# Kernel tuning notes

Hardware: AMD Instinct MI355X
Metric: run time of the kernel (lower is better)

The kernel has to match this reference:

```python
import jax, jax.numpy as jnp
import numpy as np
from jax import lax

DIM = 64
DSTATE = 16
EXPAND = 2
DINNER = DIM * EXPAND
DTRANK = (DIM + 15) // 16  # ceil(d_model/16) = 4
B, D, H, W = 1, 24, 24, 24
EPS = 1e-5


def setup_inputs() -> dict:
    key = jax.random.key(0)
    ks = jax.random.split(key, 40)
    def nrm(i, shape, s=0.02):
        return jax.random.normal(ks[i], shape, jnp.float32) * s
    inp = {}
    inp['x'] = jax.random.normal(ks[0], (B, DIM, D, H, W), jnp.float32)
    # three directional view convs + instance-norm affine params
    inp['w1'] = nrm(1, (DIM, DIM, 3, 1, 1)); inp['b1'] = jnp.zeros((DIM,), jnp.float32)
    inp['g1'] = jnp.ones((DIM,), jnp.float32) + nrm(2, (DIM,)); inp['be1'] = nrm(3, (DIM,))
    inp['w2'] = nrm(4, (DIM, DIM, 1, 3, 1)); inp['b2'] = jnp.zeros((DIM,), jnp.float32)
    inp['g2'] = jnp.ones((DIM,), jnp.float32) + nrm(5, (DIM,)); inp['be2'] = nrm(6, (DIM,))
    inp['w3'] = nrm(7, (DIM, DIM, 1, 1, 3)); inp['b3'] = jnp.zeros((DIM,), jnp.float32)
    inp['g3'] = jnp.ones((DIM,), jnp.float32) + nrm(8, (DIM,)); inp['be3'] = nrm(9, (DIM,))
    # MambaUnit layernorm
    inp['ln_w'] = jnp.ones((DIM,), jnp.float32); inp['ln_b'] = jnp.zeros((DIM,), jnp.float32)
    # Mamba params (shared across the three views, as in the source)
    inp['in_proj_w'] = nrm(10, (2 * DINNER, DIM))
    inp['conv_w'] = jnp.ones((DINNER,), jnp.float32) + nrm(11, (DINNER,))  # d_conv=1 depthwise
    inp['conv_b'] = nrm(12, (DINNER,))
    inp['x_proj_w'] = nrm(13, (DTRANK + 2 * DSTATE, DINNER))
    inp['dt_w'] = nrm(14, (DINNER, DTRANK), 0.1)
    inp['dt_b'] = nrm(15, (DINNER,), 0.1)
    inp['A_log'] = jnp.log(jnp.tile(jnp.arange(1, DSTATE + 1, dtype=jnp.float32), (DINNER, 1)))
    inp['D_param'] = jnp.ones((DINNER,), jnp.float32)
    inp['out_proj_w'] = nrm(16, (DIM, DINNER))
    # fusion 1x1x1 conv + instance norm
    inp['wf'] = nrm(17, (DIM, 3 * DIM, 1, 1, 1)); inp['bf'] = jnp.zeros((DIM,), jnp.float32)
    inp['gf'] = jnp.ones((DIM,), jnp.float32) + nrm(18, (DIM,)); inp['bef'] = nrm(19, (DIM,))
    return inp


def silu(x):
    return x * jax.nn.sigmoid(x)


def conv3d(x, w, b, pad):
    out = lax.conv_general_dilated(
        x, w, (1, 1, 1), [(pad[0], pad[0]), (pad[1], pad[1]), (pad[2], pad[2])],
        dimension_numbers=('NCDHW', 'OIDHW', 'NCDHW'))
    return out + b[None, :, None, None, None]


def instance_norm(x, g, b):
    m = x.mean(axis=(2, 3, 4), keepdims=True)
    v = x.var(axis=(2, 3, 4), keepdims=True)  # biased, as in torch InstanceNorm
    return (x - m) / jnp.sqrt(v + EPS) * g[None, :, None, None, None] + b[None, :, None, None, None]


def layer_norm(x, g, b):
    m = x.mean(axis=-1, keepdims=True)
    v = x.var(axis=-1, keepdims=True)
    return (x - m) / jnp.sqrt(v + EPS) * g + b


def mamba(u, in_proj_w, conv_w, conv_b, x_proj_w, dt_w, dt_b, A_log, D_param, out_proj_w):
    # u: (B, L, d_model)
    xz = u @ in_proj_w.T                       # (B, L, 2*DINNER)
    xi, z = jnp.split(xz, 2, axis=-1)
    xi = silu(xi * conv_w + conv_b)            # d_conv=1 depthwise conv == per-channel affine
    xdbl = xi @ x_proj_w.T                     # (B, L, DTRANK + 2*DSTATE)
    dt = xdbl[..., :DTRANK]
    Bm = xdbl[..., DTRANK:DTRANK + DSTATE]
    Cm = xdbl[..., DTRANK + DSTATE:]
    dt = jax.nn.softplus(dt @ dt_w.T + dt_b)   # (B, L, DINNER)
    A = -jnp.exp(A_log)                        # (DINNER, DSTATE)
    dA = jnp.exp(dt[..., None] * A)            # (B, L, DINNER, DSTATE)
    dBx = dt[..., None] * Bm[:, :, None, :] * xi[..., None]
    def comb(c1, c2):
        a1, b1 = c1
        a2, b2 = c2
        return a1 * a2, a2 * b1 + b2
    _, h = lax.associative_scan(comb, (dA, dBx), axis=1)  # h: (B, L, DINNER, DSTATE)
    y = jnp.einsum('blin,bln->bli', h, Cm) + xi * D_param
    y = y * silu(z)
    return y @ out_proj_w.T


def mamba_unit(x5, ln_w, ln_b, mparams):
    Bb, C = x5.shape[:2]
    dims = x5.shape[2:]
    xf = jnp.transpose(x5.reshape(Bb, C, -1), (0, 2, 1))  # (B, L, C)
    xn = layer_norm(xf, ln_w, ln_b)
    y = mamba(xn, *mparams)
    return jnp.transpose(y, (0, 2, 1)).reshape(Bb, C, *dims)


def reference(x, w1, b1, g1, be1, w2, b2, g2, be2, w3, b3, g3, be3, ln_w, ln_b,
              in_proj_w, conv_w, conv_b, x_proj_w, dt_w, dt_b, A_log, D_param, out_proj_w,
              wf, bf, gf, bef):
    mparams = (in_proj_w, conv_w, conv_b, x_proj_w, dt_w, dt_b, A_log, D_param, out_proj_w)
    v1 = jax.nn.relu(instance_norm(conv3d(x, w1, b1, (1, 0, 0)), g1, be1))
    v2 = jax.nn.relu(instance_norm(conv3d(x, w2, b2, (0, 1, 0)), g2, be2))
    v3 = jax.nn.relu(instance_norm(conv3d(x, w3, b3, (0, 0, 1)), g3, be3))
    m1 = mamba_unit(v1, ln_w, ln_b, mparams)
    m2 = mamba_unit(v2, ln_w, ln_b, mparams)
    m3 = mamba_unit(v3, ln_w, ln_b, mparams)
    cat = jnp.concatenate([m1, m2, m3], axis=1)
    out = jax.nn.relu(instance_norm(conv3d(cat, wf, bf, (0, 0, 0)), gf, bef))
    return out
```

## Files before the change

kernel.cpp:

```cpp
#include <hip/hip_runtime.h>

#define LTOT 13824
#define NCH 108
#define CHL 128
#define EPSF 1e-5f

static const size_t OFF_U   = 1024;
static const size_t NU      = (size_t)3*LTOT*64;
static const size_t NXI     = (size_t)3*LTOT*128;
static const size_t NBM     = (size_t)3*LTOT*16;
static const size_t NAG     = (size_t)3*NCH*128*16;
static const size_t OFF_XIT = OFF_U   + NU;
static const size_t OFF_SZT = OFF_XIT + NXI;
static const size_t OFF_DTT = OFF_SZT + NXI;
static const size_t OFF_BMT = OFF_DTT + NXI;
static const size_t OFF_CMT = OFF_BMT + NBM;
static const size_t OFF_W2  = OFF_CMT + NBM;
static const size_t OFF_WT  = OFF_W2 + 24576;
static const size_t OFF_WI  = OFF_WT + 36864;
static const size_t OFF_AGA = OFF_U;
static const size_t OFF_AGB = OFF_U + NAG;
static const size_t OFF_SEED= OFF_U + 2*NAG;
static const size_t OFF_FIN = OFF_DTT;

__device__ __forceinline__ float sigm(float x){ return 1.f/(1.f+__expf(-x)); }
__device__ __forceinline__ float siluf(float x){ return x*sigm(x); }
__device__ __forceinline__ float softplusf(float x){
    return fmaxf(x,0.f) + log1pf(__expf(-fabsf(x)));
}

template<int CTRL>
__device__ __forceinline__ float dpp_add(float x){
    int v = __builtin_amdgcn_update_dpp(0, __float_as_int(x), CTRL, 0xf, 0xf, true);
    return x + __int_as_float(v);
}
__device__ __forceinline__ float sum16(float x){
    x = dpp_add<0xB1>(x);
    x = dpp_add<0x4E>(x);
    x = dpp_add<0x141>(x);
    x = dpp_add<0x140>(x);
    return x;
}

__global__ __launch_bounds__(256) void k_prep(const float* __restrict__ w1,
                      const float* __restrict__ w2, const float* __restrict__ w3,
                      const float* __restrict__ opw, const float* __restrict__ wf,
                      const float* __restrict__ ipw,
                      float* __restrict__ wt, float* __restrict__ w2t,
                      float* __restrict__ wi)
{
    if (blockIdx.x < 144){
        int idx = blockIdx.x*256 + threadIdx.x;
        int r = idx / 12288, rem = idx % 12288;
        int k = rem >> 6, o = rem & 63;
        const float* W = (r==0)?w1:(r==1)?w2:w3;
        wt[idx] = W[o*192 + k];
    } else if (blockIdx.x < 240){
        int idx = (blockIdx.x-144)*256 + threadIdx.x;
        int o = idx & 63, ri = idx >> 6;
        int r = ri >> 7, i = ri & 127;
        float acc = 0.f;
        for (int c2=0;c2<64;c2++)
            acc += opw[c2*128+i] * wf[o*192 + r*64 + c2];
        w2t[idx] = acc;
    } else {
        int idx = (blockIdx.x-240)*256 + threadIdx.x;
        int col = idx & 255, q = idx >> 8;
        wi[q*256 + col] = ipw[col*64 + q];
    }
}

__global__ __launch_bounds__(192) void k_conv(const float* __restrict__ x,
                       const float* __restrict__ wt,
                       const float* __restrict__ b1, const float* __restrict__ b2,
                       const float* __restrict__ b3,
                       float* __restrict__ u, float* __restrict__ ws)
{
    __shared__ __align__(16) float xs[1152];
    __shared__ __align__(16) float wl[48*64];
    __shared__ float ssum[64], ssq[64];
    const int r = blockIdx.y;
    const int row = blockIdx.x;
    const float* Bz = (r==0)?b1:(r==1)?b2:b3;
    const int tid = threadIdx.x;

    if (tid < 64){ ssum[tid]=0.f; ssq[tid]=0.f; }

    const int og = tid & 15, wg = tid >> 4;
    const int o0 = og*4, w0 = wg*2;
    float acc[4][2];
    {
        float b0 = Bz[o0], b1v = Bz[o0+1], b2v = Bz[o0+2], b3v = Bz[o0+3];
        acc[0][0]=b0;  acc[0][1]=b0;
        acc[1][0]=b1v; acc[1][1]=b1v;
        acc[2][0]=b2v; acc[2][1]=b2v;
        acc[3][0]=b3v; acc[3][1]=b3v;
    }

    const float* wtr = wt + (size_t)r*12288;
    const int d = row/24, h = row%24;

    for (int ph=0; ph<4; ph++){
        __syncthreads();
        for (int s = tid; s < 3072; s += 192)
            wl[s] = wtr[ph*3072 + s];
        for (int s = tid; s < 1152; s += 192){
            int w = s % 24; int kt = s / 24; int ic2 = kt/3, t = kt%3;
            int ic = ph*16 + ic2;
            int src = 0; bool valid = true;
            if (r==0){ int dd = d+t-1; valid = (dd>=0 && dd<24); src = (dd*24+h)*24 + w; }
            else if (r==1){ int hh = h+t-1; valid = (hh>=0 && hh<24); src = (d*24+hh)*24 + w; }
            else { int ww = w+t-1; valid = (ww>=0 && ww<24); src = row*24 + ww; }
            xs[s] = valid ? x[(size_t)ic*LTOT + src] : 0.f;
        }
        __syncthreads();
        for (int ic2=0; ic2<16; ic2++){
            #pragma unroll
            for (int t=0;t<3;t++){
                float4 wv = *(const float4*)&wl[(ic2*3+t)*64 + o0];
                float2 xv = *(const float2*)&xs[(ic2*3+t)*24 + w0];
                acc[0][0]=fmaf(wv.x,xv.x,acc[0][0]); acc[0][1]=fmaf(wv.x,xv.y,acc[0][1]);
                acc[1][0]=fmaf(wv.y,xv.x,acc[1][0]); acc[1][1]=fmaf(wv.y,xv.y,acc[1][1]);
                acc[2][0]=fmaf(wv.z,xv.x,acc[2][0]); acc[2][1]=fmaf(wv.z,xv.y,acc[2][1]);
                acc[3][0]=fmaf(wv.w,xv.x,acc[3][0]); acc[3][1]=fmaf(wv.w,xv.y,acc[3][1]);
            }
        }
    }

    size_t ub = ((size_t)r*LTOT + (size_t)row*24)*64;
    float ps[4], pq[4];
    #pragma unroll
    for (int wj=0; wj<2; wj++){
        float4 v = make_float4(acc[0][wj],acc[1][wj],acc[2][wj],acc[3][wj]);
        *(float4*)&u[ub + (size_t)(w0+wj)*64 + o0] = v;
        if (wj==0){ ps[0]=v.x; pq[0]=v.x*v.x; ps[1]=v.y; pq[1]=v.y*v.y;
                    ps[2]=v.z; pq[2]=v.z*v.z; ps[3]=v.w; pq[3]=v.w*v.w; }
        else { ps[0]+=v.x; pq[0]+=v.x*v.x; ps[1]+=v.y; pq[1]+=v.y*v.y;
               ps[2]+=v.z; pq[2]+=v.z*v.z; ps[3]+=v.w; pq[3]+=v.w*v.w; }
    }
    #pragma unroll
    for (int oj=0;oj<4;oj++){
        atomicAdd(&ssum[o0+oj], ps[oj]);
        atomicAdd(&ssq[o0+oj], pq[oj]);
    }
    __syncthreads();
    if (tid < 64){
        atomicAdd(&ws[r*64 + tid], ssum[tid]);
        atomicAdd(&ws[192 + r*64 + tid], ssq[tid]);
    }
}

__global__ __launch_bounds__(192) void k_stats1(float* ws){
    int t = threadIdx.x;
    float s = ws[t], q = ws[192+t];
    float m = s*(1.f/(float)LTOT);
    float v = q*(1.f/(float)LTOT) - m*m;
    ws[512+t] = m; ws[704+t] = rsqrtf(v + EPSF);
}

__global__ __launch_bounds__(256, 4) void k_inproj(const float* __restrict__ u, float* __restrict__ xiT,
                         float* __restrict__ szT, const float* __restrict__ wi,
                         const float* __restrict__ cw, const float* __restrict__ cb,
                         const float* __restrict__ ws,
                         const float* g1,const float* be1,const float* g2,const float* be2,
                         const float* g3,const float* be3,
                         const float* lnw,const float* lnb)
{
    __shared__ float xl[64*65];
    const int tid = threadIdx.x, r = blockIdx.y;
    const int lane = tid & 63;
    const int wv = __builtin_amdgcn_readfirstlane(tid >> 6);
    const int l0 = blockIdx.x*64;
    size_t gbase = (size_t)r*LTOT + l0;

    {
        const float* g  = (r==0)?g1:(r==1)?g2:g3;
        const float* be = (r==0)?be1:(r==1)?be2:be3;
        float m  = ws[512 + r*64 + lane], rs = ws[704 + r*64 + lane];
        float gg = g[lane], bb = be[lane];
        float lw = lnw[lane], lb = lnb[lane];
        for (int j=0;j<16;j++){
            int p = wv*16 + j;
            float vv = u[(gbase+p)*64 + lane];
            vv = fmaxf((vv-m)*rs*gg + bb, 0.f);
            float s1 = sum16(vv), s2 = sum16(vv*vv);
            s1 += __shfl_xor(s1,16); s2 += __shfl_xor(s2,16);
            s1 += __shfl_xor(s1,32); s2 += __shfl_xor(s2,32);
            float mean = s1*(1.f/64.f);
            float var  = s2*(1.f/64.f) - mean*mean;
            xl[lane*65 + p] = (vv-mean)*rsqrtf(var+EPSF)*lw + lb;
        }
    }
    __syncthreads();

    float acc[64];
    #pragma unroll
    for (int j=0;j<64;j++) acc[j] = 0.f;
    const float* wbase = wi + wv*64;
    for (int q=0;q<64;q++){
        float xq = xl[q*65 + lane];
        const float* wq = wbase + q*256;
        #pragma unroll
        for (int j=0;j<64;j++)
            acc[j] = fmaf(wq[j], xq, acc[j]);
    }

    const bool isx = (wv < 2);
    float* dst = isx ? xiT : szT;
    const int c0 = (wv & 1)*64;
    #pragma unroll
    for (int j=0;j<64;j++){
        int c2 = c0 + j;
        float v;
        if (isx) v = siluf(fmaf(acc[j], cw[c2], cb[c2]));
        else     v = siluf(acc[j]);
        dst[((size_t)r*128 + c2)*LTOT + l0 + lane] = v;
    }
}

__global__ __launch_bounds__(256) void k_xproj(const float* __restrict__ xiT, float* __restrict__ dtT,
                        float* __restrict__ BmT, float* __restrict__ CmT,
                        const float* __restrict__ xpw, const float* __restrict__ dtw,
                        const float* __restrict__ dtb)
{
    __shared__ __align__(16) float xt[128*36];
    __shared__ float ww[36*129];
    __shared__ float sd[4*36];
    const int tid = threadIdx.x, r = blockIdx.y;
    const int l0 = blockIdx.x*32;

    for (int s = tid; s < 4096; s += 256){
        int c = s>>5, p = s&31;
        xt[c*36+p] = xiT[((size_t)r*128 + c)*LTOT + l0 + p];
    }
    for (int s = tid; s < 4608; s += 256){
        int k = s>>7, c = s&127;
        ww[k*129+c] = xpw[s];
    }
    __syncthreads();

    const int wv = tid>>6, lane = tid&63;
    float acc[8] = {0,0,0,0,0,0,0,0};
    if (lane < 36){
        const float* wrow = &ww[lane*129];
        for (int c=0;c<128;c++){
            float w = wrow[c];
            float4 a = *(const float4*)&xt[c*36 + wv*8];
            float4 b = *(const float4*)&xt[c*36 + wv*8 + 4];
            acc[0]=fmaf(w,a.x,acc[0]); acc[1]=fmaf(w,a.y,acc[1]);
            acc[2]=fmaf(w,a.z,acc[2]); acc[3]=fmaf(w,a.w,acc[3]);
            acc[4]=fmaf(w,b.x,acc[4]); acc[5]=fmaf(w,b.y,acc[5]);
            acc[6]=fmaf(w,b.z,acc[6]); acc[7]=fmaf(w,b.w,acc[7]);
        }
    }
    if (lane>=4 && lane<36){
        float* dst = (lane<20) ? BmT : CmT;
        int n = (lane<20) ? (lane-4) : (lane-20);
        size_t base = ((size_t)r*16 + n)*LTOT + l0 + wv*8;
        *(float4*)&dst[base]   = make_float4(acc[0],acc[1],acc[2],acc[3]);
        *(float4*)&dst[base+4] = make_float4(acc[4],acc[5],acc[6],acc[7]);
    }
    if (lane < 4){
        #pragma unroll
        for (int p=0;p<8;p++) sd[lane*36 + wv*8 + p] = acc[p];
    }
    __syncthreads();

    const int i = tid>>1, ph = tid&1;
    float4 dw = *(const float4*)&dtw[i*4];
    float db = dtb[i];
    float buf[16];
    #pragma unroll
    for (int t=0;t<16;t++){
        int p = ph*16 + t;
        float v = db + dw.x*sd[0*36+p] + dw.y*sd[1*36+p]
                     + dw.z*sd[2*36+p] + dw.w*sd[3*36+p];
        buf[t] = softplusf(v);
    }
    size_t base = ((size_t)r*128 + i)*LTOT + l0 + ph*16;
    #pragma unroll
    for (int q=0;q<4;q++){
        *(float4*)&dtT[base + 4*q] =
            make_float4(buf[4*q], buf[4*q+1], buf[4*q+2], buf[4*q+3]);
    }
}

__global__ __launch_bounds__(256) void k_scan1(const float* __restrict__ dtT, const float* __restrict__ BmT,
                        const float* __restrict__ xiT, const float* __restrict__ Alog,
                        float* __restrict__ aga, float* __restrict__ agb)
{
    __shared__ __align__(16) float sdt[64*68];
    __shared__ __align__(16) float sxi[64*68];
    __shared__ __align__(16) float sbm[16*68];
    const int tid = threadIdx.x;
    const int ng = tid & 3, il = tid >> 2;
    const int c = blockIdx.x, ib = blockIdx.y, r = blockIdx.z;
    const int i = ib*64 + il;

    float A2[4];
    #pragma unroll
    for (int k=0;k<4;k++) A2[k] = -expf(Alog[i*16 + ng*4 + k]) * 1.44269504f;

    const size_t rowDX = ((size_t)r*128 + ib*64)*LTOT + (size_t)c*CHL;
    const size_t rowB  = ((size_t)r*16)*LTOT + (size_t)c*CHL;

    float b0=0.f,b1=0.f,b2=0.f,b3=0.f, dsum=0.f;

    for (int hh=0; hh<2; hh++){
        __syncthreads();
        const int lb = hh*64;
        for (int f = tid; f < 1024; f += 256){
            int row = f >> 4, t4 = f & 15;
            *(float4*)&sdt[row*68 + t4*4] = *(const float4*)&dtT[rowDX + (size_t)row*LTOT + lb + t4*4];
            *(float4*)&sxi[row*68 + t4*4] = *(const float4*)&xiT[rowDX + (size_t)row*LTOT + lb + t4*4];
        }
        for (int f = tid; f < 256; f += 256){
            int row = f >> 4, t4 = f & 15;
            *(float4*)&sbm[row*68 + t4*4] = *(const float4*)&BmT[rowB + (size_t)row*LTOT + lb + t4*4];
        }
        __syncthreads();

        for (int t4 = 0; t4 < 16; t4++){
            float4 d4 = *(const float4*)&sdt[il*68 + t4*4];
            float4 x4 = *(const float4*)&sxi[il*68 + t4*4];
            float4 B0 = *(const float4*)&sbm[(ng*4+0)*68 + t4*4];
            float4 B1 = *(const float4*)&sbm[(ng*4+1)*68 + t4*4];
            float4 B2 = *(const float4*)&sbm[(ng*4+2)*68 + t4*4];
            float4 B3 = *(const float4*)&sbm[(ng*4+3)*68 + t4*4];
            #define S1Q(dv,xv,c0,c1,c2,c3) { \
                float dx = (dv)*(xv); dsum += (dv); \
                b0 = fmaf(exp2f(A2[0]*(dv)), b0, dx*(c0)); \
                b1 = fmaf(exp2f(A2[1]*(dv)), b1, dx*(c1)); \
                b2 = fmaf(exp2f(A2[2]*(dv)), b2, dx*(c2)); \
                b3 = fmaf(exp2f(A2[3]*(dv)), b3, dx*(c3)); }
            S1Q(d4.x, x4.x, B0.x, B1.x, B2.x, B3.x)
            S1Q(d4.y, x4.y, B0.y, B1.y, B2.y, B3.y)
            S1Q(d4.z, x4.z, B0.z, B1.z, B2.z, B3.z)
            S1Q(d4.w, x4.w, B0.w, B1.w, B2.w, B3.w)
            #undef S1Q
        }
    }

    size_t o = ((size_t)(r*NCH+c)*128 + i)*16 + ng*4;
    *(float4*)&aga[o] = make_float4(exp2f(A2[0]*dsum), exp2f(A2[1]*dsum),
                                    exp2f(A2[2]*dsum), exp2f(A2[3]*dsum));
    *(float4*)&agb[o] = make_float4(b0,b1,b2,b3);
}

__global__ __launch_bounds__(512) void k_scan2(const float* __restrict__ aga, const float* __restrict__ agb,
                        float* __restrict__ seed)
{
    int t = blockIdx.x*512 + threadIdx.x;
    int r = t >> 11, rem = t & 2047;
    float h = 0.f;
    for (int c=0;c<NCH;c++){
        size_t idx = (size_t)(r*NCH+c)*2048 + rem;
        float a = aga[idx], b = agb[idx];
        seed[idx] = h;
        h = fmaf(a, h, b);
    }
}

__global__ __launch_bounds__(256) void k_scan3(const float* __restrict__ dtT, const float* __restrict__ BmT,
                        const float* __restrict__ CmT, const float* __restrict__ xiT,
                        float* __restrict__ szT, const float* __restrict__ Alog,
                        const float* __restrict__ Dp, const float* __restrict__ seed)
{
    __shared__ __align__(16) float sdt[64*68];
    __shared__ __align__(16) float sxi[64*68];
    __shared__ __align__(16) float sbm[16*68];
    __shared__ __align__(16) float scm[16*68];
    const int tid = threadIdx.x;
    const int ng = tid & 3, il = tid >> 2;
    const int c = blockIdx.x, ib = blockIdx.y, r = blockIdx.z;
    const int i = ib*64 + il;

    float A2[4];
    #pragma unroll
    for (int k=0;k<4;k++) A2[k] = -expf(Alog[i*16 + ng*4 + k]) * 1.44269504f;
    const float Dv = Dp[i];

    float4 h4 = *(const float4*)&seed[((size_t)(r*NCH+c)*128 + i)*16 + ng*4];
    float h0=h4.x, h1=h4.y, h2=h4.z, h3=h4.w;

    const size_t rowDX = ((size_t)r*128 + ib*64)*LTOT + (size_t)c*CHL;
    const size_t rowB  = ((size_t)r*16)*LTOT + (size_t)c*CHL;

    for (int hh=0; hh<2; hh++){
        __syncthreads();
        const int lb = hh*64;
        for (int f = tid; f < 1024; f += 256){
            int row = f >> 4, t4 = f & 15;
            *(float4*)&sdt[row*68 + t4*4] = *(const float4*)&dtT[rowDX + (size_t)row*LTOT + lb + t4*4];
            *(float4*)&sxi[row*68 + t4*4] = *(const float4*)&xiT[rowDX + (size_t)row*LTOT + lb + t4*4];
        }
        for (int f = tid; f < 512; f += 256){
            int half = f >> 8, f2 = f & 255;
            int row = f2 >> 4, t4 = f2 & 15;
            if (half == 0)
                *(float4*)&sbm[row*68 + t4*4] = *(const float4*)&BmT[rowB + (size_t)row*LTOT + lb + t4*4];
            else
                *(float4*)&scm[row*68 + t4*4] = *(const float4*)&CmT[rowB + (size_t)row*LTOT + lb + t4*4];
        }
        __syncthreads();

        for (int t4 = 0; t4 < 16; t4++){
            float4 d4 = *(const float4*)&sdt[il*68 + t4*4];
            float4 x4 = *(const float4*)&sxi[il*68 + t4*4];
            float4 B0 = *(const float4*)&sbm[(ng*4+0)*68 + t4*4];
            float4 B1 = *(const float4*)&sbm[(ng*4+1)*68 + t4*4];
            float4 B2 = *(const float4*)&sbm[(ng*4+2)*68 + t4*4];
            float4 B3 = *(const float4*)&sbm[(ng*4+3)*68 + t4*4];
            float4 C0 = *(const float4*)&scm[(ng*4+0)*68 + t4*4];
            float4 C1 = *(const float4*)&scm[(ng*4+1)*68 + t4*4];
            float4 C2 = *(const float4*)&scm[(ng*4+2)*68 + t4*4];
            float4 C3 = *(const float4*)&scm[(ng*4+3)*68 + t4*4];
            float4 y4;
            #define S3Q(dv,xv,b0c,b1c,b2c,b3c,c0c,c1c,c2c,c3c,oy) { \
                float dx = (dv)*(xv); \
                h0 = fmaf(exp2f(A2[0]*(dv)), h0, dx*(b0c)); \
                h1 = fmaf(exp2f(A2[1]*(dv)), h1, dx*(b1c)); \
                h2 = fmaf(exp2f(A2[2]*(dv)), h2, dx*(b2c)); \
                h3 = fmaf(exp2f(A2[3]*(dv)), h3, dx*(b3c)); \
                float p = h0*(c0c); p = fmaf(h1,(c1c),p); \
                p = fmaf(h2,(c2c),p); p = fmaf(h3,(c3c),p); \
                p = dpp_add<0xB1>(p); p = dpp_add<0x4E>(p); \
                oy = fmaf((xv), Dv, p); }
            S3Q(d4.x,x4.x, B0.x,B1.x,B2.x,B3.x, C0.x,C1.x,C2.x,C3.x, y4.x)
            S3Q(d4.y,x4.y, B0.y,B1.y,B2.y,B3.y, C0.y,C1.y,C2.y,C3.y, y4.y)
            S3Q(d4.z,x4.z, B0.z,B1.z,B2.z,B3.z, C0.z,C1.z,C2.z,C3.z, y4.z)
            S3Q(d4.w,x4.w, B0.w,B1.w,B2.w,B3.w, C0.w,C1.w,C2.w,C3.w, y4.w)
            #undef S3Q
            if (ng == 0) *(float4*)&sdt[il*68 + t4*4] = y4;
        }
        __syncthreads();

        for (int f = tid; f < 1024; f += 256){
            int row = f >> 4, t4 = f & 15;
            size_t gidx = rowDX + (size_t)row*LTOT + lb + t4*4;
            float4 yv = *(const float4*)&sdt[row*68 + t4*4];
            float4 s  = *(const float4*)&szT[gidx];
            *(float4*)&szT[gidx] = make_float4(yv.x*s.x, yv.y*s.y, yv.z*s.z, yv.w*s.w);
        }
    }
}

__global__ __launch_bounds__(256, 1) void k_fin(const float* __restrict__ yT, const float* __restrict__ w2t,
                      const float* __restrict__ bfb, float* __restrict__ fin,
                      float* __restrict__ ws)
{
    __shared__ __align__(16) float yl[384*20];
    __shared__ float part[4*16*64];
    __shared__ float ssum[64], ssq[64];
    const int tid = threadIdx.x;
    const int l0 = blockIdx.x*16;
    const int o = tid & 63, sg = tid >> 6;

    for (int f = tid; f < 6144; f += 256){
        int k = f >> 4, p = f & 15;
        yl[k*20 + p] = yT[(size_t)k*LTOT + l0 + p];
    }
    float wreg[96];
    {
        const float* wp = w2t + (size_t)(sg*96)*64 + o;
        #pragma unroll
        for (int j=0;j<96;j++) wreg[j] = wp[(size_t)j*64];
    }
    if (tid < 64){ ssum[tid]=0.f; ssq[tid]=0.f; }
    __syncthreads();

    float acc[16];
    #pragma unroll
    for (int p=0;p<16;p++) acc[p]=0.f;
    const float* ylbase = &yl[sg*96*20];
    #pragma unroll
    for (int j=0;j<96;j++){
        float w = wreg[j];
        const float4* yp4 = (const float4*)&ylbase[j*20];
        float4 a = yp4[0], b = yp4[1], c = yp4[2], d = yp4[3];
        acc[0] =fmaf(w,a.x,acc[0]);  acc[1] =fmaf(w,a.y,acc[1]);
        acc[2] =fmaf(w,a.z,acc[2]);  acc[3] =fmaf(w,a.w,acc[3]);
        acc[4] =fmaf(w,b.x,acc[4]);  acc[5] =fmaf(w,b.y,acc[5]);
        acc[6] =fmaf(w,b.z,acc[6]);  acc[7] =fmaf(w,b.w,acc[7]);
        acc[8] =fmaf(w,c.x,acc[8]);  acc[9] =fmaf(w,c.y,acc[9]);
        acc[10]=fmaf(w,c.z,acc[10]); acc[11]=fmaf(w,c.w,acc[11]);
        acc[12]=fmaf(w,d.x,acc[12]); acc[13]=fmaf(w,d.y,acc[13]);
        acc[14]=fmaf(w,d.z,acc[14]); acc[15]=fmaf(w,d.w,acc[15]);
    }
    #pragma unroll
    for (int p=0;p<16;p++) part[(sg*16+p)*64 + o] = acc[p];
    __syncthreads();

    float bias = bfb[o];
    float ps=0.f, pq=0.f;
    #pragma unroll
    for (int j=0;j<4;j++){
        int p = sg + j*4;
        float s = part[(0*16+p)*64+o] + part[(1*16+p)*64+o]
                + part[(2*16+p)*64+o] + part[(3*16+p)*64+o] + bias;
        fin[(size_t)(l0+p)*64 + o] = s;
        ps += s; pq += s*s;
    }
    atomicAdd(&ssum[o], ps); atomicAdd(&ssq[o], pq);
    __syncthreads();
    if (tid<64){
        atomicAdd(&ws[384+tid], ssum[tid]);
        atomicAdd(&ws[448+tid], ssq[tid]);
    }
}

__global__ __launch_bounds__(64) void k_statsF(float* ws){
    int t = threadIdx.x;
    float s = ws[384+t], q = ws[448+t];
    float m = s*(1.f/(float)LTOT);
    float v = q*(1.f/(float)LTOT) - m*m;
    ws[896+t] = m; ws[960+t] = rsqrtf(v + EPSF);
}

__global__ __launch_bounds__(256) void k_out(const float* __restrict__ fin, const float* __restrict__ ws,
                      const float* __restrict__ gf, const float* __restrict__ bef,
                      float* __restrict__ out)
{
    __shared__ float tl[64*65];
    const int tid = threadIdx.x;
    const int l0 = blockIdx.x*64;
    for (int s=tid; s<4096; s+=256){
        int li = s>>6, o = s&63;
        float v = fin[(size_t)(l0+li)*64 + o];
        v = fmaxf((v - ws[896+o])*ws[960+o]*gf[o] + bef[o], 0.f);
        tl[o*65+li] = v;
    }
    __syncthreads();
    for (int s=tid; s<4096; s+=256){
        int o = s>>6, li = s&63;
        out[(size_t)o*LTOT + l0 + li] = tl[o*65+li];
    }
}

extern "C" void kernel_launch(void* const* d_in, const int* in_sizes, int n_in,
                              void* d_out, int out_size, void* d_ws, size_t ws_size,
                              hipStream_t stream)
{
    const float* X    = (const float*)d_in[0];
    const float* W1   = (const float*)d_in[1];  const float* B1  = (const float*)d_in[2];
    const float* G1   = (const float*)d_in[3];  const float* BE1 = (const float*)d_in[4];
    const float* W2   = (const float*)d_in[5];  const float* B2  = (const float*)d_in[6];
    const float* G2   = (const float*)d_in[7];  const float* BE2 = (const float*)d_in[8];
    const float* W3   = (const float*)d_in[9];  const float* B3  = (const float*)d_in[10];
    const float* G3   = (const float*)d_in[11]; const float* BE3 = (const float*)d_in[12];
    const float* LNW  = (const float*)d_in[13]; const float* LNB = (const float*)d_in[14];
    const float* IPW  = (const float*)d_in[15];
    const float* CW   = (const float*)d_in[16]; const float* CB  = (const float*)d_in[17];
    const float* XPW  = (const float*)d_in[18];
    const float* DTW  = (const float*)d_in[19]; const float* DTB = (const float*)d_in[20];
    const float* ALOG = (const float*)d_in[21]; const float* DP  = (const float*)d_in[22];
    const float* OPW  = (const float*)d_in[23];
    const float* WF   = (const float*)d_in[24]; const float* BF  = (const float*)d_in[25];
    const float* GF   = (const float*)d_in[26]; const float* BEF = (const float*)d_in[27];
    float* ws = (float*)d_ws;

    (void)hipMemsetAsync(d_ws, 0, 2048, stream);

    k_prep  <<<304, 256, 0, stream>>>(W1, W2, W3, OPW, WF, IPW,
                                      ws+OFF_WT, ws+OFF_W2, ws+OFF_WI);
    k_conv  <<<dim3(576,3), 192, 0, stream>>>(X, ws+OFF_WT, B1, B2, B3, ws+OFF_U, ws);
    k_stats1<<<1, 192, 0, stream>>>(ws);
    k_inproj<<<dim3(216,3), 256, 0, stream>>>(ws+OFF_U, ws+OFF_XIT, ws+OFF_SZT,
                                              ws+OFF_WI, CW, CB, ws,
                                              G1,BE1,G2,BE2,G3,BE3, LNW,LNB);
    k_xproj <<<dim3(432,3), 256, 0, stream>>>(ws+OFF_XIT, ws+OFF_DTT, ws+OFF_BMT,
                                              ws+OFF_CMT, XPW, DTW, DTB);
    k_scan1 <<<dim3(NCH,2,3), 256, 0, stream>>>(ws+OFF_DTT, ws+OFF_BMT, ws+OFF_XIT,
                                                ALOG, ws+OFF_AGA, ws+OFF_AGB);
    k_scan2 <<<12, 512, 0, stream>>>(ws+OFF_AGA, ws+OFF_AGB, ws+OFF_SEED);
    k_scan3 <<<dim3(NCH,2,3), 256, 0, stream>>>(ws+OFF_DTT, ws+OFF_BMT, ws+OFF_CMT,
                                                ws+OFF_XIT, ws+OFF_SZT, ALOG, DP,
                                                ws+OFF_SEED);
    k_fin   <<<864, 256, 0, stream>>>(ws+OFF_SZT, ws+OFF_W2, BF, ws+OFF_FIN, ws);
    k_statsF<<<1, 64, 0, stream>>>(ws);
    k_out   <<<216, 256, 0, stream>>>(ws+OFF_FIN, ws, GF, BEF, (float*)d_out);
}
```

Baseline: 378.3 us.

## Process four rows per conv block with 8x4 register tiles

The directional conv kernel now has each 192-thread block handle four output rows instead of one. Each thread computes an 8-channel by 4-position register tile, which cuts the grid from 576x3 to 144x3 blocks. This amortizes the per-block weight staging into LDS across four rows and raises FMA work per LDS load. In exchange LDS use and register pressure grow, a launch-bounds occupancy hint is added, and far fewer blocks are available to fill the GPU.

```diff
diff --git a/kernel.cpp b/kernel.cpp
--- a/kernel.cpp
+++ b/kernel.cpp
@@ -70,76 +70,97 @@
     }
 }
 
-__global__ __launch_bounds__(192) void k_conv(const float* __restrict__ x,
+__global__ __launch_bounds__(192, 3) void k_conv(const float* __restrict__ x,
                        const float* __restrict__ wt,
                        const float* __restrict__ b1, const float* __restrict__ b2,
                        const float* __restrict__ b3,
                        float* __restrict__ u, float* __restrict__ ws)
 {
-    __shared__ __align__(16) float xs[1152];
+    __shared__ __align__(16) float xs[4*1152];
     __shared__ __align__(16) float wl[48*64];
     __shared__ float ssum[64], ssq[64];
     const int r = blockIdx.y;
-    const int row = blockIdx.x;
+    const int row0 = blockIdx.x*4;
     const float* Bz = (r==0)?b1:(r==1)?b2:b3;
     const int tid = threadIdx.x;
 
     if (tid < 64){ ssum[tid]=0.f; ssq[tid]=0.f; }
 
-    const int og = tid & 15, wg = tid >> 4;
-    const int o0 = og*4, w0 = wg*2;
-    float acc[4][2];
-    {
-        float b0 = Bz[o0], b1v = Bz[o0+1], b2v = Bz[o0+2], b3v = Bz[o0+3];
-        acc[0][0]=b0;  acc[0][1]=b0;
-        acc[1][0]=b1v; acc[1][1]=b1v;
-        acc[2][0]=b2v; acc[2][1]=b2v;
-        acc[3][0]=b3v; acc[3][1]=b3v;
+    const int rw = tid / 48, t2 = tid % 48;
+    const int og = t2 & 7, wg = t2 >> 3;
+    const int o0 = og*8, w0 = wg*4;
+    const int row = row0 + rw;
+    float acc[8][4];
+    #pragma unroll
+    for (int oj=0;oj<8;oj++){
+        float b = Bz[o0+oj];
+        acc[oj][0]=b; acc[oj][1]=b; acc[oj][2]=b; acc[oj][3]=b;
     }
 
     const float* wtr = wt + (size_t)r*12288;
-    const int d = row/24, h = row%24;
+    const float* xrow = &xs[rw*1152];
 
     for (int ph=0; ph<4; ph++){
         __syncthreads();
         for (int s = tid; s < 3072; s += 192)
             wl[s] = wtr[ph*3072 + s];
-        for (int s = tid; s < 1152; s += 192){
+        for (int f = tid; f < 4608; f += 192){
+            int rw2 = f / 1152, s = f % 1152;
             int w = s % 24; int kt = s / 24; int ic2 = kt/3, t = kt%3;
             int ic = ph*16 + ic2;
+            int rr = row0 + rw2;
+            int d = rr/24, h = rr%24;
             int src = 0; bool valid = true;
             if (r==0){ int dd = d+t-1; valid = (dd>=0 && dd<24); src = (dd*24+h)*24 + w; }
             else if (r==1){ int hh = h+t-1; valid = (hh>=0 && hh<24); src = (d*24+hh)*24 + w; }
-            else { int ww = w+t-1; valid = (ww>=0 && ww<24); src = row*24 + ww; }
-            xs[s] = valid ? x[(size_t)ic*LTOT + src] : 0.f;
+            else { int ww = w+t-1; valid = (ww>=0 && ww<24); src = rr*24 + ww; }
+            xs[rw2*1152 + s] = valid ? x[(size_t)ic*LTOT + src] : 0.f;
         }
         __syncthreads();
         for (int ic2=0; ic2<16; ic2++){
             #pragma unroll
             for (int t=0;t<3;t++){
-                float4 wv = *(const float4*)&wl[(ic2*3+t)*64 + o0];
-                float2 xv = *(const float2*)&xs[(ic2*3+t)*24 + w0];
-                acc[0][0]=fmaf(wv.x,xv.x,acc[0][0]); acc[0][1]=fmaf(wv.x,xv.y,acc[0][1]);
-                acc[1][0]=fmaf(wv.y,xv.x,acc[1][0]); acc[1][1]=fmaf(wv.y,xv.y,acc[1][1]);
-                acc[2][0]=fmaf(wv.z,xv.x,acc[2][0]); acc[2][1]=fmaf(wv.z,xv.y,acc[2][1]);
-                acc[3][0]=fmaf(wv.w,xv.x,acc[3][0]); acc[3][1]=fmaf(wv.w,xv.y,acc[3][1]);
+                const int kk = ic2*3+t;
+                float4 wa = *(const float4*)&wl[kk*64 + o0];
+                float4 wb = *(const float4*)&wl[kk*64 + o0 + 4];
+                float4 xv = *(const float4*)&xrow[kk*24 + w0];
+                acc[0][0]=fmaf(wa.x,xv.x,acc[0][0]); acc[0][1]=fmaf(wa.x,xv.y,acc[0][1]);
+                acc[0][2]=fmaf(wa.x,xv.z,acc[0][2]); acc[0][3]=fmaf(wa.x,xv.w,acc[0][3]);
+                acc[1][0]=fmaf(wa.y,xv.x,acc[1][0]); acc[1][1]=fmaf(wa.y,xv.y,acc[1][1]);
+                acc[1][2]=fmaf(wa.y,xv.z,acc[1][2]); acc[1][3]=fmaf(wa.y,xv.w,acc[1][3]);
+                acc[2][0]=fmaf(wa.z,xv.x,acc[2][0]); acc[2][1]=fmaf(wa.z,xv.y,acc[2][1]);
+                acc[2][2]=fmaf(wa.z,xv.z,acc[2][2]); acc[2][3]=fmaf(wa.z,xv.w,acc[2][3]);
+                acc[3][0]=fmaf(wa.w,xv.x,acc[3][0]); acc[3][1]=fmaf(wa.w,xv.y,acc[3][1]);
+                acc[3][2]=fmaf(wa.w,xv.z,acc[3][2]); acc[3][3]=fmaf(wa.w,xv.w,acc[3][3]);
+                acc[4][0]=fmaf(wb.x,xv.x,acc[4][0]); acc[4][1]=fmaf(wb.x,xv.y,acc[4][1]);
+                acc[4][2]=fmaf(wb.x,xv.z,acc[4][2]); acc[4][3]=fmaf(wb.x,xv.w,acc[4][3]);
+                acc[5][0]=fmaf(wb.y,xv.x,acc[5][0]); acc[5][1]=fmaf(wb.y,xv.y,acc[5][1]);
+                acc[5][2]=fmaf(wb.y,xv.z,acc[5][2]); acc[5][3]=fmaf(wb.y,xv.w,acc[5][3]);
+                acc[6][0]=fmaf(wb.z,xv.x,acc[6][0]); acc[6][1]=fmaf(wb.z,xv.y,acc[6][1]);
+                acc[6][2]=fmaf(wb.z,xv.z,acc[6][2]); acc[6][3]=fmaf(wb.z,xv.w,acc[6][3]);
+                acc[7][0]=fmaf(wb.w,xv.x,acc[7][0]); acc[7][1]=fmaf(wb.w,xv.y,acc[7][1]);
+                acc[7][2]=fmaf(wb.w,xv.z,acc[7][2]); acc[7][3]=fmaf(wb.w,xv.w,acc[7][3]);
             }
         }
     }
 
     size_t ub = ((size_t)r*LTOT + (size_t)row*24)*64;
-    float ps[4], pq[4];
-    #pragma unroll
-    for (int wj=0; wj<2; wj++){
-        float4 v = make_float4(acc[0][wj],acc[1][wj],acc[2][wj],acc[3][wj]);
-        *(float4*)&u[ub + (size_t)(w0+wj)*64 + o0] = v;
-        if (wj==0){ ps[0]=v.x; pq[0]=v.x*v.x; ps[1]=v.y; pq[1]=v.y*v.y;
-                    ps[2]=v.z; pq[2]=v.z*v.z; ps[3]=v.w; pq[3]=v.w*v.w; }
-        else { ps[0]+=v.x; pq[0]+=v.x*v.x; ps[1]+=v.y; pq[1]+=v.y*v.y;
-               ps[2]+=v.z; pq[2]+=v.z*v.z; ps[3]+=v.w; pq[3]+=v.w*v.w; }
-    }
-    #pragma unroll
-    for (int oj=0;oj<4;oj++){
+    float ps[8], pq[8];
+    #pragma unroll
+    for (int oj=0;oj<8;oj++){ ps[oj]=0.f; pq[oj]=0.f; }
+    #pragma unroll
+    for (int wj=0; wj<4; wj++){
+        float4 va = make_float4(acc[0][wj],acc[1][wj],acc[2][wj],acc[3][wj]);
+        float4 vb = make_float4(acc[4][wj],acc[5][wj],acc[6][wj],acc[7][wj]);
+        *(float4*)&u[ub + (size_t)(w0+wj)*64 + o0]     = va;
+        *(float4*)&u[ub + (size_t)(w0+wj)*64 + o0 + 4] = vb;
+        ps[0]+=va.x; pq[0]+=va.x*va.x; ps[1]+=va.y; pq[1]+=va.y*va.y;
+        ps[2]+=va.z; pq[2]+=va.z*va.z; ps[3]+=va.w; pq[3]+=va.w*va.w;
+        ps[4]+=vb.x; pq[4]+=vb.x*vb.x; ps[5]+=vb.y; pq[5]+=vb.y*vb.y;
+        ps[6]+=vb.z; pq[6]+=vb.z*vb.z; ps[7]+=vb.w; pq[7]+=vb.w*vb.w;
+    }
+    #pragma unroll
+    for (int oj=0;oj<8;oj++){
         atomicAdd(&ssum[o0+oj], ps[oj]);
         atomicAdd(&ssq[o0+oj], pq[oj]);
     }
@@ -563,7 +584,7 @@
 
     k_prep  <<<304, 256, 0, stream>>>(W1, W2, W3, OPW, WF, IPW,
                                       ws+OFF_WT, ws+OFF_W2, ws+OFF_WI);
-    k_conv  <<<dim3(576,3), 192, 0, stream>>>(X, ws+OFF_WT, B1, B2, B3, ws+OFF_U, ws);
+    k_conv  <<<dim3(144,3), 192, 0, stream>>>(X, ws+OFF_WT, B1, B2, B3, ws+OFF_U, ws);
     k_stats1<<<1, 192, 0, stream>>>(ws);
     k_inproj<<<dim3(216,3), 256, 0, stream>>>(ws+OFF_U, ws+OFF_XIT, ws+OFF_SZT,
                                               ws+OFF_WI, CW, CB, ws,
```

New measurement: 387.3 us. +2.4%, slower.
